# Kernel optimization log

Hardware: AMD Instinct MI355X
Metric: run time of the kernel (lower is better)

## Reference

```python
import jax, jax.numpy as jnp
import numpy as np

NUM_NODES = 80000
NUM_EDGES = 1280000
NUM_GRAPHS = 512
IN_DIM = 64
HID = 64
NUM_CLASSES = 10


def setup_inputs() -> dict:
    key = jax.random.key(0)
    ks = jax.random.split(key, 16)
    x = jax.random.normal(ks[0], (NUM_NODES, IN_DIM), dtype=jnp.float32)
    edge_index = jax.random.randint(ks[1], (2, NUM_EDGES), 0, NUM_NODES, dtype=jnp.int64)
    batch = jnp.sort(jax.random.randint(ks[2], (NUM_NODES,), 0, NUM_GRAPHS, dtype=jnp.int64))

    def glorot(k, shape):
        fan_in, fan_out = shape[1], shape[0]
        lim = jnp.sqrt(6.0 / (fan_in + fan_out))
        return jax.random.uniform(k, shape, dtype=jnp.float32, minval=-lim, maxval=lim)

    inp = {
        "x": x,
        "edge_index": edge_index,
        "batch": batch,
        # GraphConv layer 1: lin_rel (with bias) applied to aggregated neighbors, lin_root (no bias)
        "w_rel1": glorot(ks[3], (HID, IN_DIM)),
        "b_rel1": jnp.zeros((HID,), dtype=jnp.float32),
        "w_root1": glorot(ks[4], (HID, IN_DIM)),
        # layer 2
        "w_rel2": glorot(ks[5], (HID, HID)),
        "b_rel2": jnp.zeros((HID,), dtype=jnp.float32),
        "w_root2": glorot(ks[6], (HID, HID)),
        # layer 3
        "w_rel3": glorot(ks[7], (HID, HID)),
        "b_rel3": jnp.zeros((HID,), dtype=jnp.float32),
        "w_root3": glorot(ks[8], (HID, HID)),
        # final linear head
        "w_lin": glorot(ks[9], (NUM_CLASSES, HID)),
        "b_lin": jnp.zeros((NUM_CLASSES,), dtype=jnp.float32),
    }
    return inp


def _graph_conv(x, src, dst, w_rel, b_rel, w_root):
    # PyG GraphConv with aggr='add': out_i = W_rel @ (sum_{j in N(i)} x_j) + b_rel + W_root @ x_i
    agg = jax.ops.segment_sum(x[src], dst, num_segments=NUM_NODES)  # [N, d_in]
    return agg @ w_rel.T + b_rel + x @ w_root.T


def reference(x, edge_index, batch,
              w_rel1, b_rel1, w_root1,
              w_rel2, b_rel2, w_root2,
              w_rel3, b_rel3, w_root3,
              w_lin, b_lin):
    src, dst = edge_index[0], edge_index[1]
    h = jax.nn.relu(_graph_conv(x, src, dst, w_rel1, b_rel1, w_root1))
    h = jax.nn.relu(_graph_conv(h, src, dst, w_rel2, b_rel2, w_root2))
    h = _graph_conv(h, src, dst, w_rel3, b_rel3, w_root3)
    # global_mean_pool over graph ids
    sums = jax.ops.segment_sum(h, batch, num_segments=NUM_GRAPHS)          # [G, HID]
    counts = jax.ops.segment_sum(jnp.ones((h.shape[0],), h.dtype), batch, num_segments=NUM_GRAPHS)
    pooled = sums / jnp.maximum(counts, 1.0)[:, None]
    # dropout p=0.5 is identity at inference (training=False)
    return pooled @ w_lin.T + b_lin  # [G, NUM_CLASSES]
```

## Files before the change

### kernel.cpp

```cpp
#include <hip/hip_runtime.h>

#define N_NODES  80000
#define N_EDGES  1280000
#define N_GRAPHS 512
#define DIM      64
#define NCLS     10

#define ETILE    2048
#define NTILE    625
#define NCB      625
#define BSH      7
#define HPAD     640

typedef _Float16 half8f __attribute__((ext_vector_type(8)));
typedef float float4f __attribute__((ext_vector_type(4)));

static __device__ __forceinline__ unsigned short f2h(float f) {
    _Float16 h = (_Float16)f;
    return __builtin_bit_cast(unsigned short, h);
}
static __device__ __forceinline__ float h_lo(unsigned v) {
    return (float)__builtin_bit_cast(_Float16, (unsigned short)(v & 0xFFFF));
}
static __device__ __forceinline__ float h_hi(unsigned v) {
    return (float)__builtin_bit_cast(_Float16, (unsigned short)(v >> 16));
}

__global__ __launch_bounds__(256) void k_histprep(const int* __restrict__ ei,
        const float* __restrict__ x,
        const float* __restrict__ wr1, const float* __restrict__ wo1,
        const float* __restrict__ wr2, const float* __restrict__ wo2,
        int* __restrict__ hmat, unsigned short* __restrict__ xb,
        unsigned short* __restrict__ wf) {
    __shared__ int hist[NCB];
    int bid = blockIdx.x, t = threadIdx.x;
    if (bid < NTILE) {
        int tile = bid;
        for (int i = t; i < NCB; i += 256) hist[i] = 0;
        __syncthreads();
        int base = tile * ETILE;
        int end = base + ETILE;
        for (int i = base + t; i < end; i += 256)
            atomicAdd(&hist[ei[N_EDGES + i] >> BSH], 1);
        __syncthreads();
        for (int i = t; i < NCB; i += 256) hmat[tile * HPAD + i] = hist[i];
        return;
    }
    int pb = bid - NTILE;
    if (pb < 5000) {
        int i = pb * 256 + t;
        float4 v = ((const float4*)x)[i];
        ushort4 o;
        o.x = f2h(v.x); o.y = f2h(v.y); o.z = f2h(v.z); o.w = f2h(v.w);
        ((ushort4*)xb)[i] = o;
    } else {
        int idx = (pb - 5000) * 256 + t;
        int j = idx & 7, lane = (idx >> 3) & 63;
        int ks = (idx >> 9) & 3, nt = (idx >> 11) & 3, l = idx >> 13;
        int k = ks * 32 + ((lane >> 4) & 3) * 8 + j;
        int n = nt * 16 + (lane & 15);
        const float* wr = (l == 0) ? wr1 : wr2;
        const float* wo = (l == 0) ? wo1 : wo2;
        float val = (k < 64) ? wr[n * 64 + k] : wo[n * 64 + (k - 64)];
        wf[idx] = f2h(val);
    }
}

__global__ __launch_bounds__(256) void k_scanT(const int* __restrict__ hmat,
        int* __restrict__ obase, int* __restrict__ btot) {
    __shared__ int sa[256], sb[256];
    int b = blockIdx.x, t = threadIdx.x;
    int j0 = 3 * t;
    int l0 = (j0     < NTILE) ? hmat[(j0    ) * HPAD + b] : 0;
    int l1 = (j0 + 1 < NTILE) ? hmat[(j0 + 1) * HPAD + b] : 0;
    int l2 = (j0 + 2 < NTILE) ? hmat[(j0 + 2) * HPAD + b] : 0;
    int s = l0 + l1 + l2;
    sa[t] = s; __syncthreads();
    int* sp = sa; int* dp = sb;
    for (int off = 1; off < 256; off <<= 1) {
        dp[t] = sp[t] + ((t >= off) ? sp[t - off] : 0);
        __syncthreads();
        int* tmp = sp; sp = dp; dp = tmp;
    }
    int ex = sp[t] - s;
    if (j0     < NTILE) obase[(j0    ) * HPAD + b] = ex;
    if (j0 + 1 < NTILE) obase[(j0 + 1) * HPAD + b] = ex + l0;
    if (j0 + 2 < NTILE) obase[(j0 + 2) * HPAD + b] = ex + l0 + l1;
    if (t == 255) btot[b] = sp[255];
}

__global__ __launch_bounds__(256) void k_scanB(const int* __restrict__ btot,
        int* __restrict__ bucketbase, int* __restrict__ rowptr) {
    __shared__ int sa[256], sb[256];
    int t = threadIdx.x;
    int b0 = t * 5;
    int v0 = (b0     < NCB) ? btot[b0]     : 0;
    int v1 = (b0 + 1 < NCB) ? btot[b0 + 1] : 0;
    int v2 = (b0 + 2 < NCB) ? btot[b0 + 2] : 0;
    int v3 = (b0 + 3 < NCB) ? btot[b0 + 3] : 0;
    int v4 = (b0 + 4 < NCB) ? btot[b0 + 4] : 0;
    int s = v0 + v1 + v2 + v3 + v4;
    sa[t] = s; __syncthreads();
    int* sp = sa; int* dp = sb;
    for (int off = 1; off < 256; off <<= 1) {
        dp[t] = sp[t] + ((t >= off) ? sp[t - off] : 0);
        __syncthreads();
        int* tmp = sp; sp = dp; dp = tmp;
    }
    int ex = sp[t] - s;
    if (b0     < NCB) bucketbase[b0]     = ex;
    if (b0 + 1 < NCB) bucketbase[b0 + 1] = ex + v0;
    if (b0 + 2 < NCB) bucketbase[b0 + 2] = ex + v0 + v1;
    if (b0 + 3 < NCB) bucketbase[b0 + 3] = ex + v0 + v1 + v2;
    if (b0 + 4 < NCB) bucketbase[b0 + 4] = ex + v0 + v1 + v2 + v3;
    if (t == 0) { bucketbase[NCB] = N_EDGES; rowptr[N_NODES] = N_EDGES; }
}

__global__ __launch_bounds__(256) void k_scatter2(const int* __restrict__ ei,
        const int* __restrict__ obase, const int* __restrict__ bucketbase,
        int* __restrict__ ebuf) {
    __shared__ int cur[NCB];
    int tile = blockIdx.x, t = threadIdx.x;
    for (int i = t; i < NCB; i += 256)
        cur[i] = bucketbase[i] + obase[tile * HPAD + i];
    __syncthreads();
    int base = tile * ETILE;
    int end = base + ETILE;
    for (int i = base + t; i < end; i += 256) {
        int sv = ei[i], d = ei[N_EDGES + i];
        int p = atomicAdd(&cur[d >> BSH], 1);
        ebuf[p] = sv | ((d & 127) << 17);
    }
}

__global__ __launch_bounds__(256) void k_csr2(const int* __restrict__ ebuf,
        const int* __restrict__ bucketbase, int* __restrict__ rowptr,
        int* __restrict__ col) {
    __shared__ int cnt[128], cur[128];
    __shared__ int sa[128], sb[128];
    int b = blockIdx.x, t = threadIdx.x;
    int s = bucketbase[b], e = bucketbase[b + 1];
    if (t < 128) cnt[t] = 0;
    __syncthreads();
    for (int i = s + t; i < e; i += 256) atomicAdd(&cnt[ebuf[i] >> 17], 1);
    __syncthreads();
    if (t < 128) sa[t] = cnt[t];
    __syncthreads();
    int* sp = sa; int* dp = sb;
    for (int off = 1; off < 128; off <<= 1) {
        if (t < 128) dp[t] = sp[t] + ((t >= off) ? sp[t - off] : 0);
        __syncthreads();
        int* tmp = sp; sp = dp; dp = tmp;
    }
    if (t < 128) {
        int rowbase = s + sp[t] - cnt[t];
        cur[t] = rowbase;
        rowptr[b * 128 + t] = rowbase;
    }
    __syncthreads();
    for (int i = s + t; i < e; i += 256) {
        int pk = ebuf[i];
        int p = atomicAdd(&cur[pk >> 17], 1);
        col[p] = pk & 0x1FFFF;
    }
}

__global__ __launch_bounds__(256) void k_gatherlin(
        const unsigned short* __restrict__ Xin,
        const int* __restrict__ rowptr, const int* __restrict__ col,
        const unsigned short* __restrict__ wf, const float* __restrict__ bias,
        unsigned short* __restrict__ out, int relu) {
    __shared__ uint4 sAgg[64][9];
    const half8f* Xq = (const half8f*)Xin;
    int t = threadIdx.x, w = t >> 6, lane = t & 63;
    int e = lane >> 3, c = lane & 7;
    int nb = blockIdx.x * 64 + w * 16;
    int rp = (lane <= 16) ? rowptr[nb + lane] : 0;
    for (int n = 0; n < 16; ++n) {
        int start = __shfl(rp, n), end = __shfl(rp, n + 1);
        half8f acc = {};
        int base = start;
        for (; base + 16 <= end; base += 16) {
            int i0 = col[base + e];
            int i1 = col[base + 8 + e];
            half8f v0 = Xq[(size_t)i0 * 8 + c];
            half8f v1 = Xq[(size_t)i1 * 8 + c];
            acc = acc + v0;
            acc = acc + v1;
        }
        for (; base + 8 <= end; base += 8) {
            int i0 = col[base + e];
            acc = acc + Xq[(size_t)i0 * 8 + c];
        }
        int r = end - base;
        if (e < r) {
            int i0 = col[base + e];
            acc = acc + Xq[(size_t)i0 * 8 + c];
        }
#pragma unroll
        for (int off = 8; off < 64; off <<= 1) {
            uint4 au = __builtin_bit_cast(uint4, acc);
            uint4 bu;
            bu.x = __shfl_xor(au.x, off); bu.y = __shfl_xor(au.y, off);
            bu.z = __shfl_xor(au.z, off); bu.w = __shfl_xor(au.w, off);
            acc = acc + __builtin_bit_cast(half8f, bu);
        }
        if (e == 0) sAgg[w * 16 + n][c] = __builtin_bit_cast(uint4, acc);
    }
    int quad = lane >> 4, l15 = lane & 15;
    int m = nb + l15;
    half8f a0 = *(const half8f*)&sAgg[w * 16 + l15][quad];
    half8f a1 = *(const half8f*)&sAgg[w * 16 + l15][4 + quad];
    const half8f* xr = (const half8f*)(Xin + (size_t)m * 64);
    half8f a2 = xr[quad];
    half8f a3 = xr[4 + quad];
    int orow = nb + quad * 4;
#pragma unroll
    for (int nt = 0; nt < 4; ++nt) {
        const half8f* wp = (const half8f*)(wf + ((size_t)(nt * 4) * 64 + lane) * 8);
        half8f b0 = wp[0];
        half8f b1 = wp[64];
        half8f b2 = wp[128];
        half8f b3 = wp[192];
        float4f acc = {0.f, 0.f, 0.f, 0.f};
        acc = __builtin_amdgcn_mfma_f32_16x16x32_f16(a0, b0, acc, 0, 0, 0);
        acc = __builtin_amdgcn_mfma_f32_16x16x32_f16(a1, b1, acc, 0, 0, 0);
        acc = __builtin_amdgcn_mfma_f32_16x16x32_f16(a2, b2, acc, 0, 0, 0);
        acc = __builtin_amdgcn_mfma_f32_16x16x32_f16(a3, b3, acc, 0, 0, 0);
        float bi = bias[nt * 16 + l15];
#pragma unroll
        for (int r = 0; r < 4; ++r) {
            float v = acc[r] + bi;
            if (relu) v = fmaxf(v, 0.f);
            out[(size_t)(orow + r) * 64 + nt * 16 + l15] = f2h(v);
        }
    }
}

static __device__ __forceinline__ int lowerb(const int* a, int n, int key) {
    int lo = 0, hi = n;
    while (lo < hi) { int mid = (lo + hi) >> 1; if (a[mid] < key) lo = mid + 1; else hi = mid; }
    return lo;
}

__global__ __launch_bounds__(256) void k_gsum(const unsigned short* __restrict__ h2,
        const int* __restrict__ rowptr, const int* __restrict__ col,
        const int* __restrict__ batch, float* __restrict__ S4) {
    __shared__ float red1[4][64];
    __shared__ float red2[4][64];
    const uint4* Xq = (const uint4*)h2;
    int g = blockIdx.x >> 2, part = blockIdx.x & 3;
    int t = threadIdx.x, w = t >> 6, lane = t & 63;
    int e = lane >> 3, c = lane & 7;
    int ns = lowerb(batch, N_NODES, g);
    int ne = lowerb(batch, N_NODES, g + 1);
    int a0 = ns + (int)(((long long)(ne - ns) * part) >> 2);
    int a1 = ns + (int)(((long long)(ne - ns) * (part + 1)) >> 2);
    int es = rowptr[a0], ee = rowptr[a1];
    float acc[8] = {0.f, 0.f, 0.f, 0.f, 0.f, 0.f, 0.f, 0.f};
    int idx = es + w * 8 + e;
    for (; idx + 32 < ee; idx += 64) {
        int i0 = col[idx];
        int i1 = col[idx + 32];
        uint4 v0 = Xq[(size_t)i0 * 8 + c];
        uint4 v1 = Xq[(size_t)i1 * 8 + c];
        acc[0] += h_lo(v0.x) + h_lo(v1.x); acc[1] += h_hi(v0.x) + h_hi(v1.x);
        acc[2] += h_lo(v0.y) + h_lo(v1.y); acc[3] += h_hi(v0.y) + h_hi(v1.y);
        acc[4] += h_lo(v0.z) + h_lo(v1.z); acc[5] += h_hi(v0.z) + h_hi(v1.z);
        acc[6] += h_lo(v0.w) + h_lo(v1.w); acc[7] += h_hi(v0.w) + h_hi(v1.w);
    }
    if (idx < ee) {
        int i0 = col[idx];
        uint4 v0 = Xq[(size_t)i0 * 8 + c];
        acc[0] += h_lo(v0.x); acc[1] += h_hi(v0.x);
        acc[2] += h_lo(v0.y); acc[3] += h_hi(v0.y);
        acc[4] += h_lo(v0.z); acc[5] += h_hi(v0.z);
        acc[6] += h_lo(v0.w); acc[7] += h_hi(v0.w);
    }
    float acc2[8] = {0.f, 0.f, 0.f, 0.f, 0.f, 0.f, 0.f, 0.f};
    for (int i = a0 + w * 8 + e; i < a1; i += 32) {
        uint4 v = Xq[(size_t)i * 8 + c];
        acc2[0] += h_lo(v.x); acc2[1] += h_hi(v.x);
        acc2[2] += h_lo(v.y); acc2[3] += h_hi(v.y);
        acc2[4] += h_lo(v.z); acc2[5] += h_hi(v.z);
        acc2[6] += h_lo(v.w); acc2[7] += h_hi(v.w);
    }
#pragma unroll
    for (int off = 8; off < 64; off <<= 1) {
#pragma unroll
        for (int j = 0; j < 8; ++j) {
            acc[j]  += __shfl_xor(acc[j],  off);
            acc2[j] += __shfl_xor(acc2[j], off);
        }
    }
    if (e == 0) {
#pragma unroll
        for (int j = 0; j < 8; ++j) {
            red1[w][c * 8 + j] = acc[j];
            red2[w][c * 8 + j] = acc2[j];
        }
    }
    __syncthreads();
    if (t < 64) {
        S4[(size_t)blockIdx.x * 128 + t] =
            red1[0][t] + red1[1][t] + red1[2][t] + red1[3][t];
    } else if (t < 128) {
        int d = t - 64;
        S4[(size_t)blockIdx.x * 128 + 64 + d] =
            red2[0][d] + red2[1][d] + red2[2][d] + red2[3][d];
    }
}

__global__ __launch_bounds__(64) void k_head2(const float* __restrict__ S4,
        const int* __restrict__ batch,
        const float* __restrict__ wr3, const float* __restrict__ wo3,
        const float* __restrict__ b3,
        const float* __restrict__ wlin, const float* __restrict__ blin,
        float* __restrict__ out) {
    __shared__ float s1[64], s2[64], pl[64];
    int g = blockIdx.x, t = threadIdx.x;
    int ns = lowerb(batch, N_NODES, g);
    int ne = lowerb(batch, N_NODES, g + 1);
    float inv = 1.f / (float)((ne > ns) ? (ne - ns) : 1);
    const float* Sg = S4 + (size_t)g * 4 * 128;
    s1[t] = (Sg[t]       + Sg[128 + t]       + Sg[256 + t]       + Sg[384 + t]) * inv;
    s2[t] = (Sg[64 + t]  + Sg[192 + t]       + Sg[320 + t]       + Sg[448 + t]) * inv;
    __syncthreads();
    float acc = b3[t];
    for (int k = 0; k < 64; ++k)
        acc += s1[k] * wr3[t * 64 + k] + s2[k] * wo3[t * 64 + k];
    pl[t] = acc;
    __syncthreads();
    float myout = 0.f;
    for (int cls = 0; cls < NCLS; ++cls) {
        float vv = pl[t] * wlin[cls * 64 + t];
        for (int off = 32; off > 0; off >>= 1) vv += __shfl_xor(vv, off);
        if (t == cls) myout = vv + blin[cls];
    }
    if (t < NCLS) out[g * NCLS + t] = myout;
}

extern "C" void kernel_launch(void* const* d_in, const int* in_sizes, int n_in,
                              void* d_out, int out_size, void* d_ws, size_t ws_size,
                              hipStream_t stream) {
    const float* x     = (const float*)d_in[0];
    const int*   ei    = (const int*)d_in[1];
    const int*   batch = (const int*)d_in[2];
    const float* wr1 = (const float*)d_in[3];
    const float* b1  = (const float*)d_in[4];
    const float* wo1 = (const float*)d_in[5];
    const float* wr2 = (const float*)d_in[6];
    const float* b2  = (const float*)d_in[7];
    const float* wo2 = (const float*)d_in[8];
    const float* wr3 = (const float*)d_in[9];
    const float* b3  = (const float*)d_in[10];
    const float* wo3 = (const float*)d_in[11];
    const float* wlin = (const float*)d_in[12];
    const float* blin = (const float*)d_in[13];
    float* out = (float*)d_out;

    char* p = (char*)d_ws;
    auto alloc = [&](size_t bytes) { char* r = p; p += (bytes + 255) & ~(size_t)255; return r; };
    int*   rowptr  = (int*)alloc((N_NODES + 1) * sizeof(int));
    int*   hmat    = (int*)alloc((size_t)NTILE * HPAD * sizeof(int));
    int*   obase   = (int*)alloc((size_t)NTILE * HPAD * sizeof(int));
    int*   btot    = (int*)alloc(HPAD * sizeof(int));
    int*   bucketbase = (int*)alloc((NCB + 1) * sizeof(int));
    int*   ebuf    = (int*)alloc((size_t)N_EDGES * sizeof(int));
    int*   col     = (int*)alloc((size_t)N_EDGES * sizeof(int));
    unsigned short* wf  = (unsigned short*)alloc(2 * 8192 * sizeof(unsigned short));
    unsigned short* xbf = (unsigned short*)alloc((size_t)N_NODES * 64 * 2);
    unsigned short* hA  = (unsigned short*)alloc((size_t)N_NODES * 64 * 2);
    unsigned short* hB  = (unsigned short*)alloc((size_t)N_NODES * 64 * 2);
    float* S4      = (float*)alloc((size_t)N_GRAPHS * 4 * 128 * sizeof(float));

    k_histprep<<<NTILE + 5064, 256, 0, stream>>>(ei, x, wr1, wo1, wr2, wo2,
                                                 hmat, xbf, wf);
    k_scanT   <<<NCB,   256, 0, stream>>>(hmat, obase, btot);
    k_scanB   <<<1,     256, 0, stream>>>(btot, bucketbase, rowptr);
    k_scatter2<<<NTILE, 256, 0, stream>>>(ei, obase, bucketbase, ebuf);
    k_csr2    <<<NCB,   256, 0, stream>>>(ebuf, bucketbase, rowptr, col);

    k_gatherlin<<<N_NODES / 64, 256, 0, stream>>>(xbf, rowptr, col, wf,        b1, hA, 1);
    k_gatherlin<<<N_NODES / 64, 256, 0, stream>>>(hA,  rowptr, col, wf + 8192, b2, hB, 1);

    k_gsum <<<N_GRAPHS * 4, 256, 0, stream>>>(hB, rowptr, col, batch, S4);
    k_head2<<<N_GRAPHS,     64,  0, stream>>>(S4, batch, wr3, wo3, b3, wlin, blin, out);
}
```

Before: 238.5 us.

## Partition CSR edges by source region so gathers sweep one region at a time

The CSR build now sorts each destination bucket's edges by one of four source-node regions as well as by destination row, giving a region-major rowptr layout. The gather and pooling kernels loop over the regions, so at any moment the wavefronts tend to read from one quarter of the feature table, which is meant to improve L2 locality for the random neighbor reads. The cost is a four-times larger rowptr, a 512-entry scan in the CSR kernel, 16 live half8 accumulators per wave (more registers), and the loss of the 2-way unrolled edge loop.

```diff
diff --git a/kernel.cpp b/kernel.cpp
--- a/kernel.cpp
+++ b/kernel.cpp
@@ -11,6 +11,7 @@
 #define NCB      625
 #define BSH      7
 #define HPAD     640
+#define NREG     4
 
 typedef _Float16 half8f __attribute__((ext_vector_type(8)));
 typedef float float4f __attribute__((ext_vector_type(4)));
@@ -24,6 +25,9 @@
 }
 static __device__ __forceinline__ float h_hi(unsigned v) {
     return (float)__builtin_bit_cast(_Float16, (unsigned short)(v >> 16));
+}
+static __device__ __forceinline__ int srcreg(int s) {
+    return (int)(((unsigned long long)(unsigned)s * 54975582ull) >> 40);
 }
 
 __global__ __launch_bounds__(256) void k_histprep(const int* __restrict__ ei,
@@ -90,7 +94,7 @@
 }
 
 __global__ __launch_bounds__(256) void k_scanB(const int* __restrict__ btot,
-        int* __restrict__ bucketbase, int* __restrict__ rowptr) {
+        int* __restrict__ bucketbase) {
     __shared__ int sa[256], sb[256];
     int t = threadIdx.x;
     int b0 = t * 5;
@@ -113,7 +117,7 @@
     if (b0 + 2 < NCB) bucketbase[b0 + 2] = ex + v0 + v1;
     if (b0 + 3 < NCB) bucketbase[b0 + 3] = ex + v0 + v1 + v2;
     if (b0 + 4 < NCB) bucketbase[b0 + 4] = ex + v0 + v1 + v2 + v3;
-    if (t == 0) { bucketbase[NCB] = N_EDGES; rowptr[N_NODES] = N_EDGES; }
+    if (t == 0) bucketbase[NCB] = N_EDGES;
 }
 
 __global__ __launch_bounds__(256) void k_scatter2(const int* __restrict__ ei,
@@ -133,41 +137,51 @@
     }
 }
 
-__global__ __launch_bounds__(256) void k_csr2(const int* __restrict__ ebuf,
-        const int* __restrict__ bucketbase, int* __restrict__ rowptr,
+__global__ __launch_bounds__(256) void k_csr3(const int* __restrict__ ebuf,
+        const int* __restrict__ bucketbase, int* __restrict__ rowptrR,
         int* __restrict__ col) {
-    __shared__ int cnt[128], cur[128];
-    __shared__ int sa[128], sb[128];
+    __shared__ int cnt[512], cur[512];
+    __shared__ int sa[512], sb[512];
     int b = blockIdx.x, t = threadIdx.x;
     int s = bucketbase[b], e = bucketbase[b + 1];
-    if (t < 128) cnt[t] = 0;
-    __syncthreads();
-    for (int i = s + t; i < e; i += 256) atomicAdd(&cnt[ebuf[i] >> 17], 1);
-    __syncthreads();
-    if (t < 128) sa[t] = cnt[t];
-    __syncthreads();
-    int* sp = sa; int* dp = sb;
-    for (int off = 1; off < 128; off <<= 1) {
-        if (t < 128) dp[t] = sp[t] + ((t >= off) ? sp[t - off] : 0);
-        __syncthreads();
-        int* tmp = sp; sp = dp; dp = tmp;
-    }
-    if (t < 128) {
-        int rowbase = s + sp[t] - cnt[t];
-        cur[t] = rowbase;
-        rowptr[b * 128 + t] = rowbase;
-    }
+    cnt[t] = 0; cnt[t + 256] = 0;
     __syncthreads();
     for (int i = s + t; i < e; i += 256) {
         int pk = ebuf[i];
-        int p = atomicAdd(&cur[pk >> 17], 1);
-        col[p] = pk & 0x1FFFF;
+        int key = srcreg(pk & 0x1FFFF) * 128 + (pk >> 17);
+        atomicAdd(&cnt[key], 1);
+    }
+    __syncthreads();
+    sa[t] = cnt[t]; sa[t + 256] = cnt[t + 256];
+    __syncthreads();
+    int* sp = sa; int* dp = sb;
+    for (int off = 1; off < 512; off <<= 1) {
+        int i1 = t + 256;
+        int v0 = sp[t]  + ((t  >= off) ? sp[t  - off] : 0);
+        int v1 = sp[i1] + ((i1 >= off) ? sp[i1 - off] : 0);
+        __syncthreads();
+        dp[t] = v0; dp[i1] = v1;
+        __syncthreads();
+        int* tmp = sp; sp = dp; dp = tmp;
+    }
+    int base0 = s + sp[t] - cnt[t];
+    int base1 = s + sp[t + 256] - cnt[t + 256];
+    cur[t] = base0; cur[t + 256] = base1;
+    rowptrR[b * 512 + t]       = base0;
+    rowptrR[b * 512 + 256 + t] = base1;
+    if (b == 0 && t == 0) rowptrR[NCB * 512] = N_EDGES;
+    __syncthreads();
+    for (int i = s + t; i < e; i += 256) {
+        int pk = ebuf[i];
+        int src = pk & 0x1FFFF;
+        int p = atomicAdd(&cur[srcreg(src) * 128 + (pk >> 17)], 1);
+        col[p] = src;
     }
 }
 
 __global__ __launch_bounds__(256) void k_gatherlin(
         const unsigned short* __restrict__ Xin,
-        const int* __restrict__ rowptr, const int* __restrict__ col,
+        const int* __restrict__ rowptrR, const int* __restrict__ col,
         const unsigned short* __restrict__ wf, const float* __restrict__ bias,
         unsigned short* __restrict__ out, int relu) {
     __shared__ uint4 sAgg[64][9];
@@ -175,28 +189,27 @@
     int t = threadIdx.x, w = t >> 6, lane = t & 63;
     int e = lane >> 3, c = lane & 7;
     int nb = blockIdx.x * 64 + w * 16;
-    int rp = (lane <= 16) ? rowptr[nb + lane] : 0;
+    int rbase = (nb >> 7) * 512 + (nb & 127);
+    half8f accv[16] = {};
+    for (int rg = 0; rg < NREG; ++rg) {
+        int rp = (lane <= 16) ? rowptrR[rbase + rg * 128 + lane] : 0;
+#pragma unroll
+        for (int n = 0; n < 16; ++n) {
+            int start = __shfl(rp, n), end = __shfl(rp, n + 1);
+            int base = start;
+            for (; base + 8 <= end; base += 8) {
+                int i0 = col[base + e];
+                accv[n] = accv[n] + Xq[(size_t)i0 * 8 + c];
+            }
+            if (base + e < end) {
+                int i0 = col[base + e];
+                accv[n] = accv[n] + Xq[(size_t)i0 * 8 + c];
+            }
+        }
+    }
+#pragma unroll
     for (int n = 0; n < 16; ++n) {
-        int start = __shfl(rp, n), end = __shfl(rp, n + 1);
-        half8f acc = {};
-        int base = start;
-        for (; base + 16 <= end; base += 16) {
-            int i0 = col[base + e];
-            int i1 = col[base + 8 + e];
-            half8f v0 = Xq[(size_t)i0 * 8 + c];
-            half8f v1 = Xq[(size_t)i1 * 8 + c];
-            acc = acc + v0;
-            acc = acc + v1;
-        }
-        for (; base + 8 <= end; base += 8) {
-            int i0 = col[base + e];
-            acc = acc + Xq[(size_t)i0 * 8 + c];
-        }
-        int r = end - base;
-        if (e < r) {
-            int i0 = col[base + e];
-            acc = acc + Xq[(size_t)i0 * 8 + c];
-        }
+        half8f acc = accv[n];
 #pragma unroll
         for (int off = 8; off < 64; off <<= 1) {
             uint4 au = __builtin_bit_cast(uint4, acc);
@@ -229,10 +242,10 @@
         acc = __builtin_amdgcn_mfma_f32_16x16x32_f16(a3, b3, acc, 0, 0, 0);
         float bi = bias[nt * 16 + l15];
 #pragma unroll
-        for (int r = 0; r < 4; ++r) {
-            float v = acc[r] + bi;
+        for (int r2 = 0; r2 < 4; ++r2) {
+            float v = acc[r2] + bi;
             if (relu) v = fmaxf(v, 0.f);
-            out[(size_t)(orow + r) * 64 + nt * 16 + l15] = f2h(v);
+            out[(size_t)(orow + r2) * 64 + nt * 16 + l15] = f2h(v);
         }
     }
 }
@@ -244,7 +257,7 @@
 }
 
 __global__ __launch_bounds__(256) void k_gsum(const unsigned short* __restrict__ h2,
-        const int* __restrict__ rowptr, const int* __restrict__ col,
+        const int* __restrict__ rowptrR, const int* __restrict__ col,
         const int* __restrict__ batch, float* __restrict__ S4) {
     __shared__ float red1[4][64];
     __shared__ float red2[4][64];
@@ -252,33 +265,31 @@
     int g = blockIdx.x >> 2, part = blockIdx.x & 3;
     int t = threadIdx.x, w = t >> 6, lane = t & 63;
     int e = lane >> 3, c = lane & 7;
+    int slot = w * 8 + e;
     int ns = lowerb(batch, N_NODES, g);
     int ne = lowerb(batch, N_NODES, g + 1);
     int a0 = ns + (int)(((long long)(ne - ns) * part) >> 2);
     int a1 = ns + (int)(((long long)(ne - ns) * (part + 1)) >> 2);
-    int es = rowptr[a0], ee = rowptr[a1];
     float acc[8] = {0.f, 0.f, 0.f, 0.f, 0.f, 0.f, 0.f, 0.f};
-    int idx = es + w * 8 + e;
-    for (; idx + 32 < ee; idx += 64) {
-        int i0 = col[idx];
-        int i1 = col[idx + 32];
-        uint4 v0 = Xq[(size_t)i0 * 8 + c];
-        uint4 v1 = Xq[(size_t)i1 * 8 + c];
-        acc[0] += h_lo(v0.x) + h_lo(v1.x); acc[1] += h_hi(v0.x) + h_hi(v1.x);
-        acc[2] += h_lo(v0.y) + h_lo(v1.y); acc[3] += h_hi(v0.y) + h_hi(v1.y);
-        acc[4] += h_lo(v0.z) + h_lo(v1.z); acc[5] += h_hi(v0.z) + h_hi(v1.z);
-        acc[6] += h_lo(v0.w) + h_lo(v1.w); acc[7] += h_hi(v0.w) + h_hi(v1.w);
-    }
-    if (idx < ee) {
-        int i0 = col[idx];
-        uint4 v0 = Xq[(size_t)i0 * 8 + c];
-        acc[0] += h_lo(v0.x); acc[1] += h_hi(v0.x);
-        acc[2] += h_lo(v0.y); acc[3] += h_hi(v0.y);
-        acc[4] += h_lo(v0.z); acc[5] += h_hi(v0.z);
-        acc[6] += h_lo(v0.w); acc[7] += h_hi(v0.w);
+    int b0 = a0 >> 7, b1 = (a1 - 1) >> 7;
+    for (int rg = 0; rg < NREG; ++rg) {
+        for (int b = b0; b <= b1; ++b) {
+            int nlo = a0 - (b << 7); if (nlo < 0) nlo = 0;
+            int nhi = a1 - (b << 7); if (nhi > 128) nhi = 128;
+            int rs = rowptrR[b * 512 + rg * 128 + nlo];
+            int re = rowptrR[b * 512 + rg * 128 + nhi];
+            for (int i = rs + slot; i < re; i += 32) {
+                int src = col[i];
+                uint4 v = Xq[(size_t)src * 8 + c];
+                acc[0] += h_lo(v.x); acc[1] += h_hi(v.x);
+                acc[2] += h_lo(v.y); acc[3] += h_hi(v.y);
+                acc[4] += h_lo(v.z); acc[5] += h_hi(v.z);
+                acc[6] += h_lo(v.w); acc[7] += h_hi(v.w);
+            }
+        }
     }
     float acc2[8] = {0.f, 0.f, 0.f, 0.f, 0.f, 0.f, 0.f, 0.f};
-    for (int i = a0 + w * 8 + e; i < a1; i += 32) {
+    for (int i = a0 + slot; i < a1; i += 32) {
         uint4 v = Xq[(size_t)i * 8 + c];
         acc2[0] += h_lo(v.x); acc2[1] += h_hi(v.x);
         acc2[2] += h_lo(v.y); acc2[3] += h_hi(v.y);
@@ -361,7 +372,7 @@
 
     char* p = (char*)d_ws;
     auto alloc = [&](size_t bytes) { char* r = p; p += (bytes + 255) & ~(size_t)255; return r; };
-    int*   rowptr  = (int*)alloc((N_NODES + 1) * sizeof(int));
+    int*   rowptrR = (int*)alloc(((size_t)NCB * 512 + 1) * sizeof(int));
     int*   hmat    = (int*)alloc((size_t)NTILE * HPAD * sizeof(int));
     int*   obase   = (int*)alloc((size_t)NTILE * HPAD * sizeof(int));
     int*   btot    = (int*)alloc(HPAD * sizeof(int));
@@ -377,13 +388,13 @@
     k_histprep<<<NTILE + 5064, 256, 0, stream>>>(ei, x, wr1, wo1, wr2, wo2,
                                                  hmat, xbf, wf);
     k_scanT   <<<NCB,   256, 0, stream>>>(hmat, obase, btot);
-    k_scanB   <<<1,     256, 0, stream>>>(btot, bucketbase, rowptr);
+    k_scanB   <<<1,     256, 0, stream>>>(btot, bucketbase);
     k_scatter2<<<NTILE, 256, 0, stream>>>(ei, obase, bucketbase, ebuf);
-    k_csr2    <<<NCB,   256, 0, stream>>>(ebuf, bucketbase, rowptr, col);
-
-    k_gatherlin<<<N_NODES / 64, 256, 0, stream>>>(xbf, rowptr, col, wf,        b1, hA, 1);
-    k_gatherlin<<<N_NODES / 64, 256, 0, stream>>>(hA,  rowptr, col, wf + 8192, b2, hB, 1);
-
-    k_gsum <<<N_GRAPHS * 4, 256, 0, stream>>>(hB, rowptr, col, batch, S4);
+    k_csr3    <<<NCB,   256, 0, stream>>>(ebuf, bucketbase, rowptrR, col);
+
+    k_gatherlin<<<N_NODES / 64, 256, 0, stream>>>(xbf, rowptrR, col, wf,        b1, hA, 1);
+    k_gatherlin<<<N_NODES / 64, 256, 0, stream>>>(hA,  rowptrR, col, wf + 8192, b2, hB, 1);
+
+    k_gsum <<<N_GRAPHS * 4, 256, 0, stream>>>(hB, rowptrR, col, batch, S4);
     k_head2<<<N_GRAPHS,     64,  0, stream>>>(S4, batch, wr3, wo3, b3, wlin, blin, out);
 }
```

Result: slower. 366.6 us (+53.7%).

## Build CSR with global per-node degree atomics instead of two-pass bucket sort

Applied to the files above, without the earlier changes.

Replaces the tiled two-level bucket sort (per-tile bucket histograms, transposed scan, bucket scatter, then a per-bucket counting sort) with a direct CSR build. Per-node degrees are counted with global atomics, scanned with a block-sum, top-level and expand scan, and edges are scattered using global atomic cursors per destination. This drops the large histogram matrices and the intermediate edge buffer pass. In exchange it relies on contended global atomics, and the order of columns within a row becomes nondeterministic, which can change fp16 summation order.

```diff
diff --git a/kernel.cpp b/kernel.cpp
--- a/kernel.cpp
+++ b/kernel.cpp
@@ -8,9 +8,7 @@
 
 #define ETILE    2048
 #define NTILE    625
-#define NCB      625
-#define BSH      7
-#define HPAD     640
+#define NSCB     313
 
 typedef _Float16 half8f __attribute__((ext_vector_type(8)));
 typedef float float4f __attribute__((ext_vector_type(4)));
@@ -26,35 +24,21 @@
     return (float)__builtin_bit_cast(_Float16, (unsigned short)(v >> 16));
 }
 
-__global__ __launch_bounds__(256) void k_histprep(const int* __restrict__ ei,
+__global__ __launch_bounds__(256) void k_prepdeg(const int* __restrict__ ei,
         const float* __restrict__ x,
         const float* __restrict__ wr1, const float* __restrict__ wo1,
         const float* __restrict__ wr2, const float* __restrict__ wo2,
-        int* __restrict__ hmat, unsigned short* __restrict__ xb,
+        int* __restrict__ deg, unsigned short* __restrict__ xb,
         unsigned short* __restrict__ wf) {
-    __shared__ int hist[NCB];
     int bid = blockIdx.x, t = threadIdx.x;
-    if (bid < NTILE) {
-        int tile = bid;
-        for (int i = t; i < NCB; i += 256) hist[i] = 0;
-        __syncthreads();
-        int base = tile * ETILE;
-        int end = base + ETILE;
-        for (int i = base + t; i < end; i += 256)
-            atomicAdd(&hist[ei[N_EDGES + i] >> BSH], 1);
-        __syncthreads();
-        for (int i = t; i < NCB; i += 256) hmat[tile * HPAD + i] = hist[i];
-        return;
-    }
-    int pb = bid - NTILE;
-    if (pb < 5000) {
-        int i = pb * 256 + t;
+    if (bid < 5000) {
+        int i = bid * 256 + t;
         float4 v = ((const float4*)x)[i];
         ushort4 o;
         o.x = f2h(v.x); o.y = f2h(v.y); o.z = f2h(v.z); o.w = f2h(v.w);
         ((ushort4*)xb)[i] = o;
-    } else {
-        int idx = (pb - 5000) * 256 + t;
+    } else if (bid < 5064) {
+        int idx = (bid - 5000) * 256 + t;
         int j = idx & 7, lane = (idx >> 3) & 63;
         int ks = (idx >> 9) & 3, nt = (idx >> 11) & 3, l = idx >> 13;
         int k = ks * 32 + ((lane >> 4) & 3) * 8 + j;
@@ -63,18 +47,36 @@
         const float* wo = (l == 0) ? wo1 : wo2;
         float val = (k < 64) ? wr[n * 64 + k] : wo[n * 64 + (k - 64)];
         wf[idx] = f2h(val);
-    }
-}
-
-__global__ __launch_bounds__(256) void k_scanT(const int* __restrict__ hmat,
-        int* __restrict__ obase, int* __restrict__ btot) {
+    } else {
+        int tile = bid - 5064;
+        int base = tile * ETILE;
+        int end = base + ETILE;
+        for (int i = base + t; i < end; i += 256)
+            atomicAdd(&deg[ei[N_EDGES + i]], 1);
+    }
+}
+
+__global__ __launch_bounds__(256) void k_bsum(const int* __restrict__ deg,
+        int* __restrict__ bsum) {
+    __shared__ int sa[256];
+    int b = blockIdx.x, t = threadIdx.x;
+    int idx = b * 256 + t;
+    sa[t] = (idx < N_NODES) ? deg[idx] : 0;
+    __syncthreads();
+    for (int off = 128; off > 0; off >>= 1) {
+        if (t < off) sa[t] += sa[t + off];
+        __syncthreads();
+    }
+    if (t == 0) bsum[b] = sa[0];
+}
+
+__global__ __launch_bounds__(256) void k_btop(const int* __restrict__ bsum,
+        int* __restrict__ bbase) {
     __shared__ int sa[256], sb[256];
-    int b = blockIdx.x, t = threadIdx.x;
-    int j0 = 3 * t;
-    int l0 = (j0     < NTILE) ? hmat[(j0    ) * HPAD + b] : 0;
-    int l1 = (j0 + 1 < NTILE) ? hmat[(j0 + 1) * HPAD + b] : 0;
-    int l2 = (j0 + 2 < NTILE) ? hmat[(j0 + 2) * HPAD + b] : 0;
-    int s = l0 + l1 + l2;
+    int t = threadIdx.x;
+    int l0 = (2 * t     < NSCB) ? bsum[2 * t]     : 0;
+    int l1 = (2 * t + 1 < NSCB) ? bsum[2 * t + 1] : 0;
+    int s = l0 + l1;
     sa[t] = s; __syncthreads();
     int* sp = sa; int* dp = sb;
     for (int off = 1; off < 256; off <<= 1) {
@@ -83,85 +85,41 @@
         int* tmp = sp; sp = dp; dp = tmp;
     }
     int ex = sp[t] - s;
-    if (j0     < NTILE) obase[(j0    ) * HPAD + b] = ex;
-    if (j0 + 1 < NTILE) obase[(j0 + 1) * HPAD + b] = ex + l0;
-    if (j0 + 2 < NTILE) obase[(j0 + 2) * HPAD + b] = ex + l0 + l1;
-    if (t == 255) btot[b] = sp[255];
-}
-
-__global__ __launch_bounds__(256) void k_scanB(const int* __restrict__ btot,
-        int* __restrict__ bucketbase, int* __restrict__ rowptr) {
+    if (2 * t     < NSCB) bbase[2 * t]     = ex;
+    if (2 * t + 1 < NSCB) bbase[2 * t + 1] = ex + l0;
+}
+
+__global__ __launch_bounds__(256) void k_expand(const int* __restrict__ deg,
+        const int* __restrict__ bbase, int* __restrict__ rowptr,
+        int* __restrict__ cur) {
     __shared__ int sa[256], sb[256];
-    int t = threadIdx.x;
-    int b0 = t * 5;
-    int v0 = (b0     < NCB) ? btot[b0]     : 0;
-    int v1 = (b0 + 1 < NCB) ? btot[b0 + 1] : 0;
-    int v2 = (b0 + 2 < NCB) ? btot[b0 + 2] : 0;
-    int v3 = (b0 + 3 < NCB) ? btot[b0 + 3] : 0;
-    int v4 = (b0 + 4 < NCB) ? btot[b0 + 4] : 0;
-    int s = v0 + v1 + v2 + v3 + v4;
-    sa[t] = s; __syncthreads();
+    int b = blockIdx.x, t = threadIdx.x;
+    int idx = b * 256 + t;
+    int v = (idx < N_NODES) ? deg[idx] : 0;
+    sa[t] = v; __syncthreads();
     int* sp = sa; int* dp = sb;
     for (int off = 1; off < 256; off <<= 1) {
         dp[t] = sp[t] + ((t >= off) ? sp[t - off] : 0);
         __syncthreads();
         int* tmp = sp; sp = dp; dp = tmp;
     }
-    int ex = sp[t] - s;
-    if (b0     < NCB) bucketbase[b0]     = ex;
-    if (b0 + 1 < NCB) bucketbase[b0 + 1] = ex + v0;
-    if (b0 + 2 < NCB) bucketbase[b0 + 2] = ex + v0 + v1;
-    if (b0 + 3 < NCB) bucketbase[b0 + 3] = ex + v0 + v1 + v2;
-    if (b0 + 4 < NCB) bucketbase[b0 + 4] = ex + v0 + v1 + v2 + v3;
-    if (t == 0) { bucketbase[NCB] = N_EDGES; rowptr[N_NODES] = N_EDGES; }
-}
-
-__global__ __launch_bounds__(256) void k_scatter2(const int* __restrict__ ei,
-        const int* __restrict__ obase, const int* __restrict__ bucketbase,
-        int* __restrict__ ebuf) {
-    __shared__ int cur[NCB];
+    if (idx < N_NODES) {
+        int rb = bbase[b] + sp[t] - v;
+        rowptr[idx] = rb;
+        cur[idx] = rb;
+    }
+    if (b == 0 && t == 0) rowptr[N_NODES] = N_EDGES;
+}
+
+__global__ __launch_bounds__(256) void k_scatter3(const int* __restrict__ ei,
+        int* __restrict__ cur, int* __restrict__ col) {
     int tile = blockIdx.x, t = threadIdx.x;
-    for (int i = t; i < NCB; i += 256)
-        cur[i] = bucketbase[i] + obase[tile * HPAD + i];
-    __syncthreads();
     int base = tile * ETILE;
     int end = base + ETILE;
     for (int i = base + t; i < end; i += 256) {
-        int sv = ei[i], d = ei[N_EDGES + i];
-        int p = atomicAdd(&cur[d >> BSH], 1);
-        ebuf[p] = sv | ((d & 127) << 17);
-    }
-}
-
-__global__ __launch_bounds__(256) void k_csr2(const int* __restrict__ ebuf,
-        const int* __restrict__ bucketbase, int* __restrict__ rowptr,
-        int* __restrict__ col) {
-    __shared__ int cnt[128], cur[128];
-    __shared__ int sa[128], sb[128];
-    int b = blockIdx.x, t = threadIdx.x;
-    int s = bucketbase[b], e = bucketbase[b + 1];
-    if (t < 128) cnt[t] = 0;
-    __syncthreads();
-    for (int i = s + t; i < e; i += 256) atomicAdd(&cnt[ebuf[i] >> 17], 1);
-    __syncthreads();
-    if (t < 128) sa[t] = cnt[t];
-    __syncthreads();
-    int* sp = sa; int* dp = sb;
-    for (int off = 1; off < 128; off <<= 1) {
-        if (t < 128) dp[t] = sp[t] + ((t >= off) ? sp[t - off] : 0);
-        __syncthreads();
-        int* tmp = sp; sp = dp; dp = tmp;
-    }
-    if (t < 128) {
-        int rowbase = s + sp[t] - cnt[t];
-        cur[t] = rowbase;
-        rowptr[b * 128 + t] = rowbase;
-    }
-    __syncthreads();
-    for (int i = s + t; i < e; i += 256) {
-        int pk = ebuf[i];
-        int p = atomicAdd(&cur[pk >> 17], 1);
-        col[p] = pk & 0x1FFFF;
+        int s = ei[i], d = ei[N_EDGES + i];
+        int p = atomicAdd(&cur[d], 1);
+        col[p] = s;
     }
 }
 
@@ -229,10 +187,10 @@
         acc = __builtin_amdgcn_mfma_f32_16x16x32_f16(a3, b3, acc, 0, 0, 0);
         float bi = bias[nt * 16 + l15];
 #pragma unroll
-        for (int r = 0; r < 4; ++r) {
-            float v = acc[r] + bi;
+        for (int r2 = 0; r2 < 4; ++r2) {
+            float v = acc[r2] + bi;
             if (relu) v = fmaxf(v, 0.f);
-            out[(size_t)(orow + r) * 64 + nt * 16 + l15] = f2h(v);
+            out[(size_t)(orow + r2) * 64 + nt * 16 + l15] = f2h(v);
         }
     }
 }
@@ -252,13 +210,14 @@
     int g = blockIdx.x >> 2, part = blockIdx.x & 3;
     int t = threadIdx.x, w = t >> 6, lane = t & 63;
     int e = lane >> 3, c = lane & 7;
+    int slot = w * 8 + e;
     int ns = lowerb(batch, N_NODES, g);
     int ne = lowerb(batch, N_NODES, g + 1);
     int a0 = ns + (int)(((long long)(ne - ns) * part) >> 2);
     int a1 = ns + (int)(((long long)(ne - ns) * (part + 1)) >> 2);
     int es = rowptr[a0], ee = rowptr[a1];
     float acc[8] = {0.f, 0.f, 0.f, 0.f, 0.f, 0.f, 0.f, 0.f};
-    int idx = es + w * 8 + e;
+    int idx = es + slot;
     for (; idx + 32 < ee; idx += 64) {
         int i0 = col[idx];
         int i1 = col[idx + 32];
@@ -278,7 +237,7 @@
         acc[6] += h_lo(v0.w); acc[7] += h_hi(v0.w);
     }
     float acc2[8] = {0.f, 0.f, 0.f, 0.f, 0.f, 0.f, 0.f, 0.f};
-    for (int i = a0 + w * 8 + e; i < a1; i += 32) {
+    for (int i = a0 + slot; i < a1; i += 32) {
         uint4 v = Xq[(size_t)i * 8 + c];
         acc2[0] += h_lo(v.x); acc2[1] += h_hi(v.x);
         acc2[2] += h_lo(v.y); acc2[3] += h_hi(v.y);
@@ -361,12 +320,11 @@
 
     char* p = (char*)d_ws;
     auto alloc = [&](size_t bytes) { char* r = p; p += (bytes + 255) & ~(size_t)255; return r; };
+    int*   deg     = (int*)alloc((size_t)N_NODES * sizeof(int));
+    int*   bsum    = (int*)alloc(NSCB * sizeof(int));
+    int*   bbase   = (int*)alloc(NSCB * sizeof(int));
     int*   rowptr  = (int*)alloc((N_NODES + 1) * sizeof(int));
-    int*   hmat    = (int*)alloc((size_t)NTILE * HPAD * sizeof(int));
-    int*   obase   = (int*)alloc((size_t)NTILE * HPAD * sizeof(int));
-    int*   btot    = (int*)alloc(HPAD * sizeof(int));
-    int*   bucketbase = (int*)alloc((NCB + 1) * sizeof(int));
-    int*   ebuf    = (int*)alloc((size_t)N_EDGES * sizeof(int));
+    int*   cur     = (int*)alloc((size_t)N_NODES * sizeof(int));
     int*   col     = (int*)alloc((size_t)N_EDGES * sizeof(int));
     unsigned short* wf  = (unsigned short*)alloc(2 * 8192 * sizeof(unsigned short));
     unsigned short* xbf = (unsigned short*)alloc((size_t)N_NODES * 64 * 2);
@@ -374,12 +332,13 @@
     unsigned short* hB  = (unsigned short*)alloc((size_t)N_NODES * 64 * 2);
     float* S4      = (float*)alloc((size_t)N_GRAPHS * 4 * 128 * sizeof(float));
 
-    k_histprep<<<NTILE + 5064, 256, 0, stream>>>(ei, x, wr1, wo1, wr2, wo2,
-                                                 hmat, xbf, wf);
-    k_scanT   <<<NCB,   256, 0, stream>>>(hmat, obase, btot);
-    k_scanB   <<<1,     256, 0, stream>>>(btot, bucketbase, rowptr);
-    k_scatter2<<<NTILE, 256, 0, stream>>>(ei, obase, bucketbase, ebuf);
-    k_csr2    <<<NCB,   256, 0, stream>>>(ebuf, bucketbase, rowptr, col);
+    hipMemsetAsync(deg, 0, (size_t)N_NODES * sizeof(int), stream);
+    k_prepdeg <<<5064 + NTILE, 256, 0, stream>>>(ei, x, wr1, wo1, wr2, wo2,
+                                                 deg, xbf, wf);
+    k_bsum    <<<NSCB,  256, 0, stream>>>(deg, bsum);
+    k_btop    <<<1,     256, 0, stream>>>(bsum, bbase);
+    k_expand  <<<NSCB,  256, 0, stream>>>(deg, bbase, rowptr, cur);
+    k_scatter3<<<NTILE, 256, 0, stream>>>(ei, cur, col);
 
     k_gatherlin<<<N_NODES / 64, 256, 0, stream>>>(xbf, rowptr, col, wf,        b1, hA, 1);
     k_gatherlin<<<N_NODES / 64, 256, 0, stream>>>(hA,  rowptr, col, wf + 8192, b2, hB, 1);
```

Measured after the change: 374.3 us. 1.57x slower.
